# Kernel tuning notes

Hardware: AMD Instinct MI355X
Metric: run time of the kernel (lower is better)

Reference implementation:

```python
import jax, jax.numpy as jnp
import numpy as np

N, M = 50000, 12
A, NBR = 128, 64  # atom_fea_len, nbr_fea_len
EPS = 1e-5


def setup_inputs() -> dict:
    key = jax.random.key(0)
    ks = jax.random.split(key, 6)
    atom_in_fea = jax.random.normal(ks[0], (N, A), dtype=jnp.float32)
    nbr_fea = jax.random.normal(ks[1], (N, M, NBR), dtype=jnp.float32)
    nbr_fea_idx = jax.random.randint(ks[2], (N, M), 0, N)
    tabulated_padding_fillter = jax.random.randint(ks[3], (N, M), 0, 2).astype(jnp.float32)
    fan_in = 2 * A + NBR
    W_fc = jax.random.normal(ks[4], (fan_in, 2 * A), dtype=jnp.float32) * (1.0 / np.sqrt(fan_in))
    b_fc = jnp.zeros((2 * A,), dtype=jnp.float32)
    gamma1 = jnp.ones((2 * A,), dtype=jnp.float32)
    beta1 = jnp.zeros((2 * A,), dtype=jnp.float32)
    gamma2 = jnp.ones((A,), dtype=jnp.float32)
    beta2 = jnp.zeros((A,), dtype=jnp.float32)
    return dict(atom_in_fea=atom_in_fea, nbr_fea=nbr_fea, nbr_fea_idx=nbr_fea_idx,
                tabulated_padding_fillter=tabulated_padding_fillter,
                W_fc=W_fc, b_fc=b_fc, gamma1=gamma1, beta1=beta1,
                gamma2=gamma2, beta2=beta2)


def reference(atom_in_fea, nbr_fea, nbr_fea_idx, tabulated_padding_fillter,
              W_fc, b_fc, gamma1, beta1, gamma2, beta2):
    n, m = nbr_fea_idx.shape
    a = atom_in_fea.shape[1]
    # gather neighbor atom features: (N, M, A)
    atom_nbr_fea = atom_in_fea[nbr_fea_idx]
    self_fea = jnp.broadcast_to(atom_in_fea[:, None, :], (n, m, a))
    total_nbr_fea = jnp.concatenate([self_fea, atom_nbr_fea, nbr_fea], axis=2)  # (N, M, 2A+NBR)
    total_gated_fea = total_nbr_fea @ W_fc + b_fc  # (N, M, 2A)

    # masked BatchNorm (training mode): stats over rows where filter == 1
    flat = total_gated_fea.reshape(-1, 2 * a)  # (N*M, 2A)
    mask = tabulated_padding_fillter.reshape(-1)  # (N*M,)
    cnt = jnp.sum(mask)
    mw = mask[:, None]
    mean1 = jnp.sum(flat * mw, axis=0) / cnt
    var1 = jnp.sum(((flat - mean1) ** 2) * mw, axis=0) / cnt  # biased, as torch BN
    normed = (flat - mean1) * jax.lax.rsqrt(var1 + EPS) * gamma1 + beta1
    flat = jnp.where(mw == 1, normed, flat)  # only masked rows replaced
    total_gated_fea = flat.reshape(n, m, 2 * a)

    nbr_filter, nbr_core = jnp.split(total_gated_fea, 2, axis=2)
    nbr_sumed = jnp.sum(jax.nn.sigmoid(nbr_filter) * jax.nn.softplus(nbr_core)
                        * tabulated_padding_fillter[:, :, None], axis=1)  # (N, A)

    # BatchNorm over all N rows (training-mode batch stats)
    mean2 = jnp.mean(nbr_sumed, axis=0)
    var2 = jnp.var(nbr_sumed, axis=0)
    nbr_sumed = (nbr_sumed - mean2) * jax.lax.rsqrt(var2 + EPS) * gamma2 + beta2

    return jax.nn.softplus(atom_in_fea + nbr_sumed)
```

## Files before the change

kernel.cpp:

```cpp
#include <hip/hip_runtime.h>

typedef unsigned short u16;
typedef unsigned int u32;

#define N_ATOM   50000
#define M_NBR    12
#define A_FEA    128
#define NBR_FEA  64
#define KDIM     320
#define CDIM     256
#define ROWS     600000
#define RPB      48
#define NBLK     12500
#define KC       10
#define EPSV     1e-5f
#define A_PITCH  656
#define GRID1    512
#define BUFSZ    31744
#define MASK_OFF 31488

using frag  = __attribute__((ext_vector_type(8))) short;
using f32x4 = __attribute__((ext_vector_type(4))) float;

#define WS_SUM1      0
#define WS_SUMSQ1    256
#define WS_CNT       512
#define WS_SUM2      516
#define WS_SUMSQ2    644
#define WS_STATS_END 772
#define WS_SCALE1    1024
#define WS_SHIFT1    1280
#define WS_NBR       2048
#define WS_W_FOFF    (2048 + 6400000)
#define WS_P_FOFF    (2048 + 6400000 + 40960)
#define WS_G_FOFF    (WS_P_FOFF + 6400000)
#define WS_NEED_BYTES 358572032ull

__device__ __forceinline__ u32 fbits(float f) { union { float f; u32 u; } v; v.f = f; return v.u; }
__device__ __forceinline__ float bits2f(u32 u) { union { u32 u; float f; } v; v.u = u; return v.f; }
__device__ __forceinline__ u32 pkbf(float a, float b) {
    return __builtin_amdgcn_perm(fbits(b) + 0x8000u, fbits(a) + 0x8000u, 0x07060302u);
}
__device__ __forceinline__ u16 f2bf1(float f) { return (u16)((fbits(f) + 0x8000u) >> 16); }
__device__ __forceinline__ float bf2f(u16 u) { return bits2f(((u32)u) << 16); }
__device__ __forceinline__ float softplusf(float x) {
    return fmaxf(x, 0.f) + __logf(1.f + __expf(-fabsf(x)));
}
__device__ __forceinline__ float sigmoidf(float x) {
    return __builtin_amdgcn_rcpf(1.f + __expf(-x));
}

__global__ void swizzleW(const float* __restrict__ W, u16* __restrict__ wsW) {
    int g = blockIdx.x * 256 + threadIdx.x;
    if (g >= KDIM * CDIM) return;
    int k = g >> 8, n = g & 255;
    u32 u = fbits(W[g]);
    u32 r = u + 0x7fffu + ((u >> 16) & 1u);
    wsW[((k >> 5) * 256 + n) * 32 + (k & 31)] = (u16)(r >> 16);
}

__global__ __launch_bounds__(256) void mask_cnt(const float* __restrict__ mask, float* __restrict__ ws) {
    int t = blockIdx.x * 256 + threadIdx.x;
    float s = 0.f;
    if (t < 37500) {
        const float* p = mask + (size_t)t * 16;
        #pragma unroll
        for (int i = 0; i < 4; i++) {
            float4 v = *(const float4*)(p + i * 4);
            s += (v.x + v.y) + (v.z + v.w);
        }
    }
    #pragma unroll
    for (int d = 1; d < 64; d <<= 1) s += __shfl_xor(s, d, 64);
    __shared__ float r[4];
    int l = threadIdx.x & 63, w = threadIdx.x >> 6;
    if (l == 0) r[w] = s;
    __syncthreads();
    if (threadIdx.x == 0) atomicAdd(&ws[WS_CNT], r[0] + r[1] + r[2] + r[3]);
}

struct Meta {
    int   idx[3];
    float mg[3];
    float mnA, mnB;
    float mrow;
};
struct Data {
    float4 sv, gv[3], nva, nvb;
};

__device__ __forceinline__ void load_meta(Meta& M, const int* __restrict__ nbridx,
                                          const float* __restrict__ mask,
                                          int r0, int w, int l, int tid) {
    const int h32 = l >> 5;
    #pragma unroll
    for (int j = 0; j < 3; ++j) {
        int row = 6 * w + 2 * j + h32;
        M.idx[j] = nbridx[r0 + row];
        M.mg[j]  = mask[r0 + row];
    }
    M.mnA = mask[r0 + 6 * w + (l >> 4)];
    M.mnB = (l < 32) ? mask[r0 + 6 * w + 4 + (l >> 4)] : 0.f;
    M.mrow = (tid < 48) ? mask[r0 + tid] : 0.f;
}

__device__ __forceinline__ void load_data(Data& D, const Meta& M,
                                          const float* __restrict__ atom,
                                          const float* __restrict__ nbrf,
                                          int t, int w, int l) {
    const int c32 = l & 31;
    D.sv = *(const float4*)(atom + (size_t)(t * 4 + (w >> 1)) * 128 + c32 * 4);
    #pragma unroll
    for (int j = 0; j < 3; ++j)
        if (M.mg[j] != 0.f)
            D.gv[j] = *(const float4*)(atom + (size_t)M.idx[j] * 128 + c32 * 4);
    const float* nb = nbrf + (size_t)(t * RPB + 6 * w) * 64;
    if (M.mnA != 0.f) D.nva = *(const float4*)(nb + (l >> 4) * 64 + (l & 15) * 4);
    if (l < 32 && M.mnB != 0.f) D.nvb = *(const float4*)(nb + (4 + (l >> 4)) * 64 + (l & 15) * 4);
}

__device__ __forceinline__ void write_tile(const Data& D, const Meta& M, char* nb,
                                           int w, int l, int tid) {
    const int h32 = l >> 5, c32 = l & 31;
    {
        uint2 p; p.x = pkbf(D.sv.x, D.sv.y); p.y = pkbf(D.sv.z, D.sv.w);
        #pragma unroll
        for (int jj = 0; jj < 3; ++jj)
            *(uint2*)(nb + (6 * w + 3 * h32 + jj) * A_PITCH + c32 * 8) = p;
    }
    #pragma unroll
    for (int j = 0; j < 3; ++j) {
        int row = 6 * w + 2 * j + h32;
        uint2 g; g.x = 0u; g.y = 0u;
        if (M.mg[j] != 0.f) { g.x = pkbf(D.gv[j].x, D.gv[j].y); g.y = pkbf(D.gv[j].z, D.gv[j].w); }
        *(uint2*)(nb + row * A_PITCH + 256 + c32 * 8) = g;
    }
    {
        int rowA = 6 * w + (l >> 4);
        uint2 na; na.x = 0u; na.y = 0u;
        if (M.mnA != 0.f) { na.x = pkbf(D.nva.x, D.nva.y); na.y = pkbf(D.nva.z, D.nva.w); }
        *(uint2*)(nb + rowA * A_PITCH + 512 + (l & 15) * 8) = na;
    }
    if (l < 32) {
        int rowB = 6 * w + 4 + (l >> 4);
        uint2 nv; nv.x = 0u; nv.y = 0u;
        if (M.mnB != 0.f) { nv.x = pkbf(D.nvb.x, D.nvb.y); nv.y = pkbf(D.nvb.z, D.nvb.w); }
        *(uint2*)(nb + rowB * A_PITCH + 512 + (l & 15) * 8) = nv;
    }
    if (tid < 48) *(float*)(nb + MASK_OFF + tid * 4) = M.mrow;
}

__global__ __launch_bounds__(512, 2) void gemm1_pipe(
    const float* __restrict__ atom, const float* __restrict__ nbrf,
    const int* __restrict__ nbridx, const float* __restrict__ mask,
    const u16* __restrict__ wsW, float* __restrict__ ws)
{
    __shared__ __align__(16) char smem[2 * BUFSZ];
    const int tid = threadIdx.x;
    const int w = tid >> 6, l = tid & 63, l15 = l & 15, l4 = l >> 4;
    u32* __restrict__ Hbase = (u32*)(ws + WS_G_FOFF);

    frag Bf[KC][2];
    #pragma unroll
    for (int kk = 0; kk < KC; ++kk)
        #pragma unroll
        for (int cf = 0; cf < 2; ++cf)
            Bf[kk][cf] = *(const frag*)((const char*)wsW +
                ((size_t)(kk * 256 + cf * 128 + 16 * w + l15) * 64 + l4 * 16));

    Meta M; Data D;
    float cnt_acc = 0.f;
    float sacc[2] = {0.f, 0.f}, qacc[2] = {0.f, 0.f};
    const int t0 = blockIdx.x;

    load_meta(M, nbridx, mask, t0 * RPB, w, l, tid);
    cnt_acc += M.mrow;
    load_data(D, M, atom, nbrf, t0, w, l);
    write_tile(D, M, smem, w, l, tid);
    if (t0 + GRID1 < NBLK) {
        load_meta(M, nbridx, mask, (t0 + GRID1) * RPB, w, l, tid);
        cnt_acc += M.mrow;
    }
    __syncthreads();

    int cur = 0;
    for (int t = t0; t < NBLK; t += GRID1) {
        const int tn = t + GRID1;
        const bool hasNext = (tn < NBLK);
        char* bufc = smem + cur * BUFSZ;
        char* bufn = smem + (cur ^ 1) * BUFSZ;

        if (hasNext) load_data(D, M, atom, nbrf, tn, w, l);

        f32x4 acc[3][2];
        #pragma unroll
        for (int rf = 0; rf < 3; ++rf) {
            acc[rf][0] = (f32x4){0.f, 0.f, 0.f, 0.f};
            acc[rf][1] = (f32x4){0.f, 0.f, 0.f, 0.f};
        }
        const char* Ac = bufc + l15 * A_PITCH + l4 * 16;
        #pragma unroll
        for (int kk = 0; kk < KC; ++kk) {
            frag a[3];
            #pragma unroll
            for (int rf = 0; rf < 3; ++rf)
                a[rf] = *(const frag*)(Ac + rf * 16 * A_PITCH + kk * 64);
            #pragma unroll
            for (int rf = 0; rf < 3; ++rf) {
                acc[rf][0] = __builtin_amdgcn_mfma_f32_16x16x32_bf16(a[rf], Bf[kk][0], acc[rf][0], 0, 0, 0);
                acc[rf][1] = __builtin_amdgcn_mfma_f32_16x16x32_bf16(a[rf], Bf[kk][1], acc[rf][1], 0, 0, 0);
            }
        }

        f32x4 mm[3];
        #pragma unroll
        for (int rf = 0; rf < 3; ++rf)
            mm[rf] = *(const f32x4*)(bufc + MASK_OFF + (rf * 16 + l4 * 4) * 4);
        #pragma unroll
        for (int cf = 0; cf < 2; ++cf) {
            float s = 0.f, q = 0.f;
            #pragma unroll
            for (int rf = 0; rf < 3; ++rf)
                #pragma unroll
                for (int rg = 0; rg < 4; ++rg) {
                    float mv = mm[rf][rg];
                    float v = acc[rf][cf][rg];
                    s += mv * v; q += mv * v * v;
                }
            s += __shfl_xor(s, 16, 64); s += __shfl_xor(s, 32, 64);
            q += __shfl_xor(q, 16, 64); q += __shfl_xor(q, 32, 64);
            sacc[cf] += s;
            qacc[cf] += q;
        }
        {
            u32* H = Hbase + (size_t)t * (RPB * 128) + 16 * w + l15;
            #pragma unroll
            for (int rf = 0; rf < 3; ++rf)
                #pragma unroll
                for (int rg = 0; rg < 4; ++rg) {
                    const int row = rf * 16 + l4 * 4 + rg;
                    if (mm[rf][rg] != 0.f)
                        H[(size_t)row * 128] = pkbf(acc[rf][0][rg], acc[rf][1][rg]);
                }
        }

        if (hasNext) write_tile(D, M, bufn, w, l, tid);
        if (tn + GRID1 < NBLK) {
            load_meta(M, nbridx, mask, (tn + GRID1) * RPB, w, l, tid);
            cnt_acc += M.mrow;
        }
        __syncthreads();
        cur ^= 1;
    }

    if (l4 == 0) {
        #pragma unroll
        for (int cf = 0; cf < 2; ++cf) {
            int col = cf * 128 + 16 * w + l15;
            atomicAdd(&ws[WS_SUM1 + col],   sacc[cf]);
            atomicAdd(&ws[WS_SUMSQ1 + col], qacc[cf]);
        }
    }
    if (w == 0) {
        float c = cnt_acc;
        #pragma unroll
        for (int d = 1; d < 64; d <<= 1) c += __shfl_xor(c, d, 64);
        if (l == 0) atomicAdd(&ws[WS_CNT], c);
    }
}

template <int MODE>
__global__ __launch_bounds__(256, 3) void gemm_pass(
    const float* __restrict__ atom, const float* __restrict__ nbrf,
    const int* __restrict__ nbridx, const float* __restrict__ mask,
    const u16* __restrict__ wsW, float* __restrict__ ws)
{
    __shared__ __align__(16) char smem[RPB * A_PITCH];
    __shared__ float m_lds[RPB];
    __shared__ int   idx_lds[RPB];
    __shared__ float red[(MODE == 2) ? 4 : 1][128];

    const int tid = threadIdx.x;
    const int w = tid >> 6, l = tid & 63, l15 = l & 15, l4 = l >> 4;
    const int h32 = l >> 5, c32 = l & 31;
    const int blk = blockIdx.x;
    const int r0 = blk * RPB;
    float* __restrict__ P = ws + WS_P_FOFF;

    if (tid < RPB) {
        m_lds[tid] = mask[r0 + tid];
        idx_lds[tid] = nbridx[r0 + tid];
    }
    __syncthreads();

    {
        float4 sv = *(const float4*)(atom + (size_t)(blk * 4 + w) * 128 + c32 * 4);
        uint2 p; p.x = pkbf(sv.x, sv.y); p.y = pkbf(sv.z, sv.w);
        #pragma unroll
        for (int jj = 0; jj < 6; ++jj) {
            int row = 12 * w + 6 * h32 + jj;
            *(uint2*)(smem + row * A_PITCH + c32 * 8) = p;
        }
    }
    {
        float4 v[6]; float mrow[6];
        #pragma unroll
        for (int i = 0; i < 6; ++i) {
            int row = 12 * w + 2 * i + h32;
            mrow[i] = m_lds[row];
            if (mrow[i] != 0.f)
                v[i] = *(const float4*)(atom + (size_t)idx_lds[row] * 128 + c32 * 4);
        }
        #pragma unroll
        for (int i = 0; i < 6; ++i) {
            int row = 12 * w + 2 * i + h32;
            uint2 p; p.x = 0u; p.y = 0u;
            if (mrow[i] != 0.f) { p.x = pkbf(v[i].x, v[i].y); p.y = pkbf(v[i].z, v[i].w); }
            *(uint2*)(smem + row * A_PITCH + 256 + c32 * 8) = p;
        }
    }
    {
        const float* nf = nbrf + (size_t)(r0 + 12 * w) * 64;
        float4 v[3]; float mrow[3]; int rowv[3], cv[3];
        #pragma unroll
        for (int i = 0; i < 3; ++i) {
            int g = i * 64 + l;
            rowv[i] = 12 * w + (g >> 4);
            cv[i] = g & 15;
            mrow[i] = m_lds[rowv[i]];
            if (mrow[i] != 0.f) v[i] = *(const float4*)(nf + g * 4);
        }
        #pragma unroll
        for (int i = 0; i < 3; ++i) {
            uint2 p; p.x = 0u; p.y = 0u;
            if (mrow[i] != 0.f) { p.x = pkbf(v[i].x, v[i].y); p.y = pkbf(v[i].z, v[i].w); }
            *(uint2*)(smem + rowv[i] * A_PITCH + 512 + cv[i] * 8) = p;
        }
    }
    __syncthreads();

    f32x4 acc[3][4];
    #pragma unroll
    for (int rf = 0; rf < 3; rf++)
        #pragma unroll
        for (int cf = 0; cf < 4; cf++)
            acc[rf][cf] = (f32x4){0.f, 0.f, 0.f, 0.f};

    const char* Ab = smem + l15 * A_PITCH + l4 * 16;
    const char* Bb = (const char*)wsW + ((size_t)w * 2048 + l15 * 64 + l4 * 16);
    frag bcur[4], bnext[4];
    #pragma unroll
    for (int cf = 0; cf < 4; ++cf)
        bcur[cf] = *(const frag*)(Bb + cf * 1024 + (cf >= 2 ? 6144 : 0));
    #pragma unroll
    for (int kk = 0; kk < KC; ++kk) {
        if (kk < KC - 1) {
            const char* Bn = Bb + (kk + 1) * 16384;
            #pragma unroll
            for (int cf = 0; cf < 4; ++cf)
                bnext[cf] = *(const frag*)(Bn + cf * 1024 + (cf >= 2 ? 6144 : 0));
        }
        frag a[3];
        #pragma unroll
        for (int rf = 0; rf < 3; rf++)
            a[rf] = *(const frag*)(Ab + rf * 16 * A_PITCH + kk * 64);
        #pragma unroll
        for (int rf = 0; rf < 3; rf++)
            #pragma unroll
            for (int cf = 0; cf < 4; cf++)
                acc[rf][cf] = __builtin_amdgcn_mfma_f32_16x16x32_bf16(a[rf], bcur[cf], acc[rf][cf], 0, 0, 0);
        #pragma unroll
        for (int cf = 0; cf < 4; ++cf) bcur[cf] = bnext[cf];
    }

    if constexpr (MODE == 0) {
        #pragma unroll
        for (int cf = 0; cf < 4; cf++) {
            float s = 0.f, q = 0.f;
            #pragma unroll
            for (int rf = 0; rf < 3; rf++)
                #pragma unroll
                for (int rg = 0; rg < 4; rg++) {
                    int row = rf * 16 + l4 * 4 + rg;
                    float mv = m_lds[row];
                    float v = acc[rf][cf][rg];
                    s += mv * v; q += mv * v * v;
                }
            s += __shfl_xor(s, 16, 64); s += __shfl_xor(s, 32, 64);
            q += __shfl_xor(q, 16, 64); q += __shfl_xor(q, 32, 64);
            if (l4 == 0) {
                int col = w * 32 + cf * 16 + (cf >= 2 ? 96 : 0) + l15;
                P[(size_t)blk * 512 + col]       = s;
                P[(size_t)blk * 512 + 256 + col] = q;
            }
        }
    } else {
        __syncthreads();
        u16* g16 = (u16*)smem;
        #pragma unroll
        for (int cf = 0; cf < 4; cf++) {
            int col = w * 32 + cf * 16 + (cf >= 2 ? 96 : 0) + l15;
            float sc = ws[WS_SCALE1 + col];
            float sh = ws[WS_SHIFT1 + col];
            #pragma unroll
            for (int rf = 0; rf < 3; rf++)
                #pragma unroll
                for (int rg = 0; rg < 4; rg++) {
                    int row = rf * 16 + l4 * 4 + rg;
                    g16[row * 256 + col] = f2bf1(acc[rf][cf][rg] * sc + sh);
                }
        }
        __syncthreads();
        int h = tid >> 7;
        int c = tid & 127;
        float ns0 = 0.f, ns1 = 0.f;
        #pragma unroll
        for (int la2 = 0; la2 < 2; la2++) {
            int la = h * 2 + la2;
            float a_ns = 0.f;
            #pragma unroll
            for (int j = 0; j < 12; j++) {
                int row = la * 12 + j;
                float f = bf2f(g16[row * 256 + c]);
                float k = bf2f(g16[row * 256 + 128 + c]);
                a_ns += m_lds[row] * sigmoidf(f) * softplusf(k);
            }
            ws[WS_NBR + (blk * 4 + la) * 128 + c] = a_ns;
            if (la2 == 0) ns0 = a_ns; else ns1 = a_ns;
        }
        red[h][c]     = ns0 + ns1;
        red[2 + h][c] = ns0 * ns0 + ns1 * ns1;
        __syncthreads();
        if (tid < 128) {
            P[(size_t)blk * 256 + tid]       = red[0][tid] + red[1][tid];
            P[(size_t)blk * 256 + 128 + tid] = red[2][tid] + red[3][tid];
        }
    }
}

__global__ __launch_bounds__(256) void pass2_gate(
    const float* __restrict__ ws_ro, const float* __restrict__ mask,
    const float* __restrict__ g1, const float* __restrict__ b1,
    float* __restrict__ ws)
{
    __shared__ float m_lds[RPB];
    __shared__ float redS[4][128];
    __shared__ float redQ[4][128];

    const int tid = threadIdx.x;
    const int blk = blockIdx.x;
    const int h = tid >> 6;
    const int lane = tid & 63;
    const int c0 = 2 * lane, c1 = 2 * lane + 1;
    float* __restrict__ P = ws + WS_P_FOFF;

    if (tid < RPB) m_lds[tid] = mask[blk * RPB + tid];

    const float rc = 1.f / ws_ro[WS_CNT];
    float scf0, shf0, sck0, shk0, scf1, shf1, sck1, shk1;
    {
        float m = ws_ro[WS_SUM1 + c0] * rc;
        float v = ws_ro[WS_SUMSQ1 + c0] * rc - m * m;
        scf0 = g1[c0] * rsqrtf(v + EPSV); shf0 = b1[c0] - m * scf0;
    }
    {
        float m = ws_ro[WS_SUM1 + 128 + c0] * rc;
        float v = ws_ro[WS_SUMSQ1 + 128 + c0] * rc - m * m;
        sck0 = g1[128 + c0] * rsqrtf(v + EPSV); shk0 = b1[128 + c0] - m * sck0;
    }
    {
        float m = ws_ro[WS_SUM1 + c1] * rc;
        float v = ws_ro[WS_SUMSQ1 + c1] * rc - m * m;
        scf1 = g1[c1] * rsqrtf(v + EPSV); shf1 = b1[c1] - m * scf1;
    }
    {
        float m = ws_ro[WS_SUM1 + 128 + c1] * rc;
        float v = ws_ro[WS_SUMSQ1 + 128 + c1] * rc - m * m;
        sck1 = g1[128 + c1] * rsqrtf(v + EPSV); shk1 = b1[128 + c1] - m * sck1;
    }
    __syncthreads();

    const uint2* Hb = (const uint2*)((const u32*)(ws_ro + WS_G_FOFF)
                        + (size_t)blk * (RPB * 128) + (size_t)(h * 12) * 128) + lane;

    uint2 v[12]; float mv[12];
    #pragma unroll
    for (int j = 0; j < 12; j++) {
        mv[j] = m_lds[h * 12 + j];
        if (mv[j] != 0.f) v[j] = Hb[j * 64];
    }
    float ns0 = 0.f, ns1 = 0.f;
    #pragma unroll
    for (int j = 0; j < 12; j++) {
        if (mv[j] != 0.f) {
            u32 ux = v[j].x, uy = v[j].y;
            float f0 = bits2f(ux << 16)          * scf0 + shf0;
            float k0 = bits2f(ux & 0xffff0000u)  * sck0 + shk0;
            float f1 = bits2f(uy << 16)          * scf1 + shf1;
            float k1 = bits2f(uy & 0xffff0000u)  * sck1 + shk1;
            ns0 += __builtin_amdgcn_rcpf(1.f + __expf(-f0)) *
                   (fmaxf(k0, 0.f) + __logf(1.f + __expf(-fabsf(k0))));
            ns1 += __builtin_amdgcn_rcpf(1.f + __expf(-f1)) *
                   (fmaxf(k1, 0.f) + __logf(1.f + __expf(-fabsf(k1))));
        }
    }
    {
        float2 o; o.x = ns0; o.y = ns1;
        *(float2*)(ws + WS_NBR + (size_t)(blk * 4 + h) * 128 + c0) = o;
    }
    redS[h][c0] = ns0; redS[h][c1] = ns1;
    redQ[h][c0] = ns0 * ns0; redQ[h][c1] = ns1 * ns1;
    __syncthreads();
    if (tid < 128) {
        P[(size_t)blk * 256 + tid]       = redS[0][tid] + redS[1][tid] + redS[2][tid] + redS[3][tid];
        P[(size_t)blk * 256 + 128 + tid] = redQ[0][tid] + redQ[1][tid] + redQ[2][tid] + redQ[3][tid];
    }
}

__global__ __launch_bounds__(256) void red1(const float* __restrict__ ws_ro, float* __restrict__ ws) {
    const float* P = ws_ro + WS_P_FOFF;
    int c = (blockIdx.x & 1) * 256 + threadIdx.x;
    int s = blockIdx.x >> 1;
    const float* p = P + (size_t)s * 100 * 512 + c;
    float a = 0.f;
    #pragma unroll 4
    for (int r = 0; r < 100; r++) a += p[(size_t)r * 512];
    atomicAdd(&ws[WS_SUM1 + c], a);
}

__global__ __launch_bounds__(256) void red2(const float* __restrict__ ws_ro, float* __restrict__ ws) {
    const float* P = ws_ro + WS_P_FOFF;
    int s = blockIdx.x;
    const float* p = P + (size_t)s * 100 * 256 + threadIdx.x;
    float a = 0.f;
    #pragma unroll 4
    for (int r = 0; r < 100; r++) a += p[(size_t)r * 256];
    atomicAdd(&ws[WS_SUM2 + threadIdx.x], a);
}

__global__ void finalize1(float* __restrict__ ws, const float* __restrict__ g1, const float* __restrict__ b1) {
    int c = threadIdx.x;
    float cnt = ws[WS_CNT];
    float mean = ws[WS_SUM1 + c] / cnt;
    float var  = ws[WS_SUMSQ1 + c] / cnt - mean * mean;
    float sc = g1[c] * rsqrtf(var + EPSV);
    ws[WS_SCALE1 + c] = sc;
    ws[WS_SHIFT1 + c] = b1[c] - mean * sc;
}

__global__ __launch_bounds__(256) void out_kernel(
    const float* __restrict__ atom, const float* __restrict__ ws,
    const float* __restrict__ g2, const float* __restrict__ b2,
    float* __restrict__ out)
{
    int g = blockIdx.x * 256 + threadIdx.x;
    if (g >= N_ATOM * 32) return;
    int i = g >> 5, c4 = (g & 31) * 4;
    const float inv = 1.f / (float)N_ATOM;
    float4 s2  = *(const float4*)(ws + WS_SUM2 + c4);
    float4 q2  = *(const float4*)(ws + WS_SUMSQ2 + c4);
    float4 g2v = *(const float4*)(g2 + c4);
    float4 b2v = *(const float4*)(b2 + c4);
    float4 sc, sh;
    { float m = s2.x * inv; sc.x = g2v.x * rsqrtf(q2.x * inv - m * m + EPSV); sh.x = b2v.x - m * sc.x; }
    { float m = s2.y * inv; sc.y = g2v.y * rsqrtf(q2.y * inv - m * m + EPSV); sh.y = b2v.y - m * sc.y; }
    { float m = s2.z * inv; sc.z = g2v.z * rsqrtf(q2.z * inv - m * m + EPSV); sh.z = b2v.z - m * sc.z; }
    { float m = s2.w * inv; sc.w = g2v.w * rsqrtf(q2.w * inv - m * m + EPSV); sh.w = b2v.w - m * sc.w; }
    float4 av = *(const float4*)(atom + i * 128 + c4);
    float4 nv = *(const float4*)(ws + WS_NBR + i * 128 + c4);
    float4 ov;
    ov.x = softplusf(av.x + nv.x * sc.x + sh.x);
    ov.y = softplusf(av.y + nv.y * sc.y + sh.y);
    ov.z = softplusf(av.z + nv.z * sc.z + sh.z);
    ov.w = softplusf(av.w + nv.w * sc.w + sh.w);
    *(float4*)(out + i * 128 + c4) = ov;
}

extern "C" void kernel_launch(void* const* d_in, const int* in_sizes, int n_in,
                              void* d_out, int out_size, void* d_ws, size_t ws_size,
                              hipStream_t stream) {
    (void)in_sizes; (void)n_in; (void)out_size;
    const float* atom = (const float*)d_in[0];
    const float* nbrf = (const float*)d_in[1];
    const int*   nidx = (const int*)d_in[2];
    const float* mask = (const float*)d_in[3];
    const float* W    = (const float*)d_in[4];
    const float* g1 = (const float*)d_in[6];
    const float* b1 = (const float*)d_in[7];
    const float* g2 = (const float*)d_in[8];
    const float* b2 = (const float*)d_in[9];
    float* ws  = (float*)d_ws;
    u16*  wsW  = (u16*)((char*)d_ws + (size_t)WS_W_FOFF * 4);
    float* out = (float*)d_out;
    const bool bigws = (ws_size >= WS_NEED_BYTES);

    hipMemsetAsync(d_ws, 0, WS_STATS_END * 4, stream);
    swizzleW<<<(KDIM * CDIM + 255) / 256, 256, 0, stream>>>(W, wsW);
    if (bigws) {
        gemm1_pipe<<<GRID1, 512, 0, stream>>>(atom, nbrf, nidx, mask, wsW, ws);
        pass2_gate<<<NBLK, 256, 0, stream>>>(ws, mask, g1, b1, ws);
        red2<<<125, 256, 0, stream>>>(ws, ws);
    } else {
        mask_cnt<<<147, 256, 0, stream>>>(mask, ws);
        gemm_pass<0><<<NBLK, 256, 0, stream>>>(atom, nbrf, nidx, mask, wsW, ws);
        red1<<<250, 256, 0, stream>>>(ws, ws);
        finalize1<<<1, 256, 0, stream>>>(ws, g1, b1);
        gemm_pass<2><<<NBLK, 256, 0, stream>>>(atom, nbrf, nidx, mask, wsW, ws);
        red2<<<125, 256, 0, stream>>>(ws, ws);
    }
    out_kernel<<<(N_ATOM * 32 + 255) / 256, 256, 0, stream>>>(atom, ws, g2, b2, out);
}
```

Measured before the change: 424.9 us.

## Make pass2 gate kernel persistent with software-prefetched tiles

```diff
diff --git a/kernel.cpp b/kernel.cpp
--- a/kernel.cpp
+++ b/kernel.cpp
@@ -16,6 +16,7 @@
 #define EPSV     1e-5f
 #define A_PITCH  656
 #define GRID1    512
+#define PG2      2048
 #define BUFSZ    31744
 #define MASK_OFF 31488
 
@@ -438,23 +439,19 @@
     }
 }
 
-__global__ __launch_bounds__(256) void pass2_gate(
+__global__ __launch_bounds__(256) void pass2_persist(
     const float* __restrict__ ws_ro, const float* __restrict__ mask,
     const float* __restrict__ g1, const float* __restrict__ b1,
     float* __restrict__ ws)
 {
-    __shared__ float m_lds[RPB];
     __shared__ float redS[4][128];
     __shared__ float redQ[4][128];
 
     const int tid = threadIdx.x;
-    const int blk = blockIdx.x;
     const int h = tid >> 6;
     const int lane = tid & 63;
-    const int c0 = 2 * lane, c1 = 2 * lane + 1;
+    const int c0 = 2 * lane, c1 = c0 + 1;
     float* __restrict__ P = ws + WS_P_FOFF;
-
-    if (tid < RPB) m_lds[tid] = mask[blk * RPB + tid];
 
     const float rc = 1.f / ws_ro[WS_CNT];
     float scf0, shf0, sck0, shk0, scf1, shf1, sck1, shk1;
@@ -478,42 +475,70 @@
         float v = ws_ro[WS_SUMSQ1 + 128 + c1] * rc - m * m;
         sck1 = g1[128 + c1] * rsqrtf(v + EPSV); shk1 = b1[128 + c1] - m * sck1;
     }
-    __syncthreads();
-
-    const uint2* Hb = (const uint2*)((const u32*)(ws_ro + WS_G_FOFF)
-                        + (size_t)blk * (RPB * 128) + (size_t)(h * 12) * 128) + lane;
-
-    uint2 v[12]; float mv[12];
-    #pragma unroll
-    for (int j = 0; j < 12; j++) {
-        mv[j] = m_lds[h * 12 + j];
-        if (mv[j] != 0.f) v[j] = Hb[j * 64];
-    }
-    float ns0 = 0.f, ns1 = 0.f;
-    #pragma unroll
-    for (int j = 0; j < 12; j++) {
-        if (mv[j] != 0.f) {
-            u32 ux = v[j].x, uy = v[j].y;
-            float f0 = bits2f(ux << 16)          * scf0 + shf0;
-            float k0 = bits2f(ux & 0xffff0000u)  * sck0 + shk0;
-            float f1 = bits2f(uy << 16)          * scf1 + shf1;
-            float k1 = bits2f(uy & 0xffff0000u)  * sck1 + shk1;
-            ns0 += __builtin_amdgcn_rcpf(1.f + __expf(-f0)) *
-                   (fmaxf(k0, 0.f) + __logf(1.f + __expf(-fabsf(k0))));
-            ns1 += __builtin_amdgcn_rcpf(1.f + __expf(-f1)) *
-                   (fmaxf(k1, 0.f) + __logf(1.f + __expf(-fabsf(k1))));
-        }
-    }
-    {
-        float2 o; o.x = ns0; o.y = ns1;
-        *(float2*)(ws + WS_NBR + (size_t)(blk * 4 + h) * 128 + c0) = o;
-    }
-    redS[h][c0] = ns0; redS[h][c1] = ns1;
-    redQ[h][c0] = ns0 * ns0; redQ[h][c1] = ns1 * ns1;
-    __syncthreads();
-    if (tid < 128) {
-        P[(size_t)blk * 256 + tid]       = redS[0][tid] + redS[1][tid] + redS[2][tid] + redS[3][tid];
-        P[(size_t)blk * 256 + 128 + tid] = redQ[0][tid] + redQ[1][tid] + redQ[2][tid] + redQ[3][tid];
+
+    const u32* H0 = (const u32*)(ws_ro + WS_G_FOFF);
+
+    float mA[12]; uint2 vA[12];
+    float mB[12];
+    const int t0 = blockIdx.x;
+
+    {
+        #pragma unroll
+        for (int j = 0; j < 12; j++) mA[j] = mask[t0 * RPB + h * 12 + j];
+        const uint2* Hb = (const uint2*)(H0 + (size_t)t0 * (RPB * 128) + (size_t)(h * 12) * 128) + lane;
+        #pragma unroll
+        for (int j = 0; j < 12; j++) if (mA[j] != 0.f) vA[j] = Hb[(size_t)j * 64];
+    }
+    if (t0 + PG2 < NBLK) {
+        #pragma unroll
+        for (int j = 0; j < 12; j++) mB[j] = mask[(t0 + PG2) * RPB + h * 12 + j];
+    }
+
+    for (int t = t0; t < NBLK; t += PG2) {
+        const int tn = t + PG2;
+
+        uint2 vB[12];
+        if (tn < NBLK) {
+            const uint2* Hn = (const uint2*)(H0 + (size_t)tn * (RPB * 128) + (size_t)(h * 12) * 128) + lane;
+            #pragma unroll
+            for (int j = 0; j < 12; j++) if (mB[j] != 0.f) vB[j] = Hn[(size_t)j * 64];
+        }
+        float mC[12];
+        if (tn + PG2 < NBLK) {
+            #pragma unroll
+            for (int j = 0; j < 12; j++) mC[j] = mask[(tn + PG2) * RPB + h * 12 + j];
+        }
+
+        float ns0 = 0.f, ns1 = 0.f;
+        #pragma unroll
+        for (int j = 0; j < 12; j++) {
+            if (mA[j] != 0.f) {
+                const u32 ux = vA[j].x, uy = vA[j].y;
+                float f0 = bits2f(ux << 16)         * scf0 + shf0;
+                float k0 = bits2f(ux & 0xffff0000u) * sck0 + shk0;
+                float f1 = bits2f(uy << 16)         * scf1 + shf1;
+                float k1 = bits2f(uy & 0xffff0000u) * sck1 + shk1;
+                ns0 += __builtin_amdgcn_rcpf(1.f + __expf(-f0)) *
+                       (fmaxf(k0, 0.f) + __logf(1.f + __expf(-fabsf(k0))));
+                ns1 += __builtin_amdgcn_rcpf(1.f + __expf(-f1)) *
+                       (fmaxf(k1, 0.f) + __logf(1.f + __expf(-fabsf(k1))));
+            }
+        }
+        {
+            float2 o; o.x = ns0; o.y = ns1;
+            *(float2*)(ws + WS_NBR + (size_t)(t * 4 + h) * 128 + c0) = o;
+        }
+        redS[h][c0] = ns0;        redS[h][c1] = ns1;
+        redQ[h][c0] = ns0 * ns0;  redQ[h][c1] = ns1 * ns1;
+        __syncthreads();
+        if (tid < 128) {
+            P[(size_t)t * 256 + tid]       = redS[0][tid] + redS[1][tid] + redS[2][tid] + redS[3][tid];
+            P[(size_t)t * 256 + 128 + tid] = redQ[0][tid] + redQ[1][tid] + redQ[2][tid] + redQ[3][tid];
+        }
+        __syncthreads();
+
+        #pragma unroll
+        for (int j = 0; j < 12; j++) { mA[j] = mB[j]; vA[j] = vB[j]; mB[j] = mC[j]; }
     }
 }
 
@@ -598,7 +623,7 @@
     swizzleW<<<(KDIM * CDIM + 255) / 256, 256, 0, stream>>>(W, wsW);
     if (bigws) {
         gemm1_pipe<<<GRID1, 512, 0, stream>>>(atom, nbrf, nidx, mask, wsW, ws);
-        pass2_gate<<<NBLK, 256, 0, stream>>>(ws, mask, g1, b1, ws);
+        pass2_persist<<<PG2, 256, 0, stream>>>(ws, mask, g1, b1, ws);
         red2<<<125, 256, 0, stream>>>(ws, ws);
     } else {
         mask_cnt<<<147, 256, 0, stream>>>(mask, ws);
```

New measurement: 427.5 us. Within noise of the previous version (+0.6%).
